# Kernel tuning notes

Hardware: AMD Instinct MI355X
Metric: run time of the kernel (lower is better)

Reference implementation:

```python
import jax, jax.numpy as jnp
import numpy as np

B, C, H, W, K = 2, 3, 256, 256, 51  # output H,W; filter size K; input is (H+K-1, W+K-1)


def _sepconv(inp, vertical, horizontal):
    # inp: [B,C,H+K-1,W+K-1]; vertical/horizontal: [B,K,H,W]
    Kf = vertical.shape[1]
    Ho, Wo = vertical.shape[2], vertical.shape[3]
    rows = jnp.stack([inp[:, :, i:i + Ho, :] for i in range(Kf)], axis=0)

    def body(acc, j):
        # window for horizontal offset j: [K,B,C,Ho,Wo]
        win = jax.lax.dynamic_slice_in_dim(rows, j, Wo, axis=4)
        # contract over vertical taps i with per-pixel vertical kernel
        vcon = jnp.einsum('kbchw,bkhw->bchw', win, vertical)
        # weight by per-pixel horizontal tap j and accumulate
        acc = acc + vcon * horizontal[:, j][:, None, :, :]
        return acc, None

    acc0 = jnp.zeros((inp.shape[0], inp.shape[1], Ho, Wo), inp.dtype)
    out, _ = jax.lax.scan(body, acc0, jnp.arange(Kf))
    return out


def setup_inputs() -> dict:
    key = jax.random.key(0)
    k1, k2, k3 = jax.random.split(key, 3)
    tenInput = jax.random.normal(k1, (B, C, H + K - 1, W + K - 1), dtype=jnp.float32)
    tenVertical = jax.random.normal(k2, (B, K, H, W), dtype=jnp.float32)
    tenHorizontal = jax.random.normal(k3, (B, K, H, W), dtype=jnp.float32)
    return {"tenInput": tenInput, "tenVertical": tenVertical, "tenHorizontal": tenHorizontal}


def reference(tenInput, tenVertical, tenHorizontal):
    return _sepconv(tenInput, tenVertical, tenHorizontal)
```

## Files before the change

kernel.cpp:

```cpp
#include <hip/hip_runtime.h>


namespace {
constexpr int KK = 51;
constexpr int NB = 2;
constexpr int NC = 3;
constexpr int HH = 256;
constexpr int WW = 256;
constexpr int IN_H = HH + KK - 1;
constexpr int IN_W = WW + KK - 1;

constexpr int TILE_W = 64;
constexpr int TILE_H = 8;
constexpr int NTX = 8;
constexpr int R = 8;
constexpr int NTY = 8;
constexpr int NS = 4;
constexpr int NTHREADS = NTX * NTY * NS;
constexpr int HALO_W = TILE_W + KK - 1;
constexpr int LDS_W = 116;
constexpr int LDS_H = TILE_H + KK - 1;
constexpr int KSTRIDE = HH * WW;
constexpr int HCH  = 4 * TILE_H * TILE_W;
constexpr int UNIT = 2 * HCH;
}

__device__ __forceinline__ float fget(const float4 v, int i) {
  return (i == 0) ? v.x : (i == 1) ? v.y : (i == 2) ? v.z : v.w;
}

template <int P, int JJ>
__device__ __forceinline__ void fma_jtap(const float4 (&v4)[4][2], const float4 (&w4)[4][3],
                                         const float4 ha, const float4 hb, float (&acc)[R]) {
#pragma unroll
  for (int rx = 0; rx < R; ++rx) {
    const int k  = rx + JJ;
    const int sl = (P + k / 4) % 3;
    const int cp = k & 3;
    const int vh = rx >> 2, vc = rx & 3;
    float tv = fget(v4[0][vh], vc) * fget(w4[0][sl], cp);
    tv = fmaf(fget(v4[1][vh], vc), fget(w4[1][sl], cp), tv);
    tv = fmaf(fget(v4[2][vh], vc), fget(w4[2][sl], cp), tv);
    tv = fmaf(fget(v4[3][vh], vc), fget(w4[3][sl], cp), tv);
    const float hv = (rx < 4) ? fget(ha, vc) : fget(hb, vc);
    acc[rx] = fmaf(hv, tv, acc[rx]);
  }
}

template <int P>
__device__ __forceinline__ void full_chunk(const float4 (&v4)[4][2], float4 (&w4)[4][3],
                                           const int (&woff)[4], int wcol,
                                           const float* hb, int off0, int off1,
                                           float (&acc)[R], const float* smem) {
  const float4 h0a = *reinterpret_cast<const float4*>(hb + off0);
  const float4 h0b = *reinterpret_cast<const float4*>(hb + off1);
  const float4 h1a = *reinterpret_cast<const float4*>(hb + 512 + off0);
  const float4 h1b = *reinterpret_cast<const float4*>(hb + 512 + off1);
  fma_jtap<P, 0>(v4, w4, h0a, h0b, acc);
  const float4 h2a = *reinterpret_cast<const float4*>(hb + 1024 + off0);
  const float4 h2b = *reinterpret_cast<const float4*>(hb + 1024 + off1);
  fma_jtap<P, 1>(v4, w4, h1a, h1b, acc);
  const float4 h3a = *reinterpret_cast<const float4*>(hb + 1536 + off0);
  const float4 h3b = *reinterpret_cast<const float4*>(hb + 1536 + off1);
  fma_jtap<P, 2>(v4, w4, h2a, h2b, acc);
  fma_jtap<P, 3>(v4, w4, h3a, h3b, acc);
#pragma unroll
  for (int ib = 0; ib < 4; ++ib)
    w4[ib][P] = *reinterpret_cast<const float4*>(&smem[woff[ib] + wcol]);
}

__global__ __launch_bounds__(NTHREADS, 1)
void sepconv_kernel(
    const float* __restrict__ inp,
    const float* __restrict__ vert,
    const float* __restrict__ horiz,
    float* __restrict__ out)
{
  __shared__ float lds[LDS_H * LDS_W];
  __shared__ float hbuf[2 * UNIT];

  const int tid = threadIdx.x;
  const int tx  = tid & (NTX - 1);
  const int ty  = (tid >> 3) & (NTY - 1);
  const int s   = tid >> 6;

  const int x0 = blockIdx.x * TILE_W;
  const int y0 = blockIdx.y * TILE_H;
  const int bc = blockIdx.z;
  const int b  = bc / NC;
  const int c  = bc % NC;

  {
    const float* src = inp + (((size_t)(b * NC + c)) * IN_H + y0) * IN_W + x0;
    constexpr int total2 = LDS_H * (HALO_W / 2);
    for (int e = tid; e < total2; e += NTHREADS) {
      const int col2 = e % (HALO_W / 2);
      const int r    = e / (HALO_W / 2);
      const float2 v = *reinterpret_cast<const float2*>(src + (size_t)r * IN_W + col2 * 2);
      float* dst = &lds[r * LDS_W + col2 * 2];
      dst[0] = v.x; dst[1] = v.y;
    }
  }

  const float* hblk = horiz + (((size_t)b * KK) * HH + y0) * WW + x0;
  int jj_[4], goff_[4], ldso_[4];
#pragma unroll
  for (int r = 0; r < 4; ++r) {
    const int p   = r * 256 + tid;
    const int rem = p & 127;
    const int row = rem >> 4;
    const int c4  = rem & 15;
    const int q   = (c4 - row) & 15;
    jj_[r]   = p >> 7;
    goff_[r] = row * WW + q * 4;
    ldso_[r] = (r * 256 + (tid & ~63)) * 4;
  }
  auto stage_full = [&](int jbase, int bufn) {
#pragma unroll
    for (int r = 0; r < 4; ++r) {
      const float* g = hblk + (size_t)(jbase + jj_[r]) * KSTRIDE + goff_[r];
      float* l = &hbuf[bufn * UNIT + ldso_[r]];
      __builtin_amdgcn_global_load_lds((const __attribute__((address_space(1))) void*)g,
                                       (__attribute__((address_space(3))) void*)l, 16, 0, 0);
    }
  };
  auto stage_half = [&](int bufn) {
#pragma unroll
    for (int r = 0; r < 2; ++r) {
      const int j  = 48 + jj_[r];
      const int jc = (j <= 50) ? j : 50;
      const float* g = hblk + (size_t)jc * KSTRIDE + goff_[r];
      float* l = &hbuf[bufn * UNIT + ldso_[r]];
      __builtin_amdgcn_global_load_lds((const __attribute__((address_space(1))) void*)g,
                                       (__attribute__((address_space(3))) void*)l, 16, 0, 0);
    }
  };

  stage_full(0, 0);
  __syncthreads();
  int buf = 0;
  int un  = 1;

  auto stage_next = [&]() {
    if (un < 6) stage_full(8 * un, buf ^ 1);
    else        stage_half(buf ^ 1);
    un = (un == 6) ? 0 : un + 1;
  };

  const int lx = tx * R;
  const int xg = x0 + lx;
  const int yg = y0 + ty;

  const int off0 = ty * 64 + ((2 * tx + ty) & 15) * 4;
  const int off1 = ty * 64 + ((2 * tx + 1 + ty) & 15) * 4;

  float acc[R];
#pragma unroll
  for (int rx = 0; rx < R; ++rx) acc[rx] = 0.f;

  const int blk0 = (s == 0) ? 0 : (3 * s + 1);
  const int nblk = (s == 0) ? 4 : 3;

  const float* vbase = vert + (((size_t)b * KK) * HH + yg) * WW + xg;

#pragma unroll 1
  for (int t = 0; t < 4; ++t) {
    const bool act = (t < nblk);
    float4 v4[4][2];
    float4 w4[4][3];
    int    woff[4];
    if (act) {
      const int ibase = (blk0 + t) * 4;
#pragma unroll
      for (int ib = 0; ib < 4; ++ib) {
        const int iv = ibase + ib;
        const int ic = (iv <= 50) ? iv : 50;
        float4 va = *reinterpret_cast<const float4*>(vbase + (size_t)ic * KSTRIDE);
        float4 vb = *reinterpret_cast<const float4*>(vbase + (size_t)ic * KSTRIDE + 4);
        if (iv > 50) { va = make_float4(0.f, 0.f, 0.f, 0.f); vb = va; }
        v4[ib][0] = va; v4[ib][1] = vb;
        woff[ib] = (ty + ic) * LDS_W;
        const float4* p = reinterpret_cast<const float4*>(&lds[woff[ib] + lx]);
        w4[ib][0] = p[0]; w4[ib][1] = p[1]; w4[ib][2] = p[2];
      }
    }

#pragma unroll 1
    for (int h2 = 0; h2 < 2; ++h2) {
      const int cb = lx + 24 * h2 + 12;
      const float* hb0;
      stage_next();
      hb0 = hbuf + buf * UNIT;
      if (act) {
        full_chunk<0>(v4, w4, woff, cb + 0, hb0,        off0, off1, acc, lds);
        full_chunk<1>(v4, w4, woff, cb + 4, hb0 + HCH,  off0, off1, acc, lds);
      }
      __syncthreads(); buf ^= 1;
      stage_next();
      hb0 = hbuf + buf * UNIT;
      if (act) {
        full_chunk<2>(v4, w4, woff, cb + 8,  hb0,       off0, off1, acc, lds);
        full_chunk<0>(v4, w4, woff, cb + 12, hb0 + HCH, off0, off1, acc, lds);
      }
      __syncthreads(); buf ^= 1;
      stage_next();
      hb0 = hbuf + buf * UNIT;
      if (act) {
        full_chunk<1>(v4, w4, woff, cb + 16, hb0,       off0, off1, acc, lds);
        full_chunk<2>(v4, w4, woff, cb + 20, hb0 + HCH, off0, off1, acc, lds);
      }
      __syncthreads(); buf ^= 1;
    }

    stage_next();
    if (act) {
      const float* hb = hbuf + buf * UNIT;
      const float4 e0a = *reinterpret_cast<const float4*>(hb + off0);
      const float4 e0b = *reinterpret_cast<const float4*>(hb + off1);
      const float4 e1a = *reinterpret_cast<const float4*>(hb + 512 + off0);
      const float4 e1b = *reinterpret_cast<const float4*>(hb + 512 + off1);
      const float4 e2a = *reinterpret_cast<const float4*>(hb + 1024 + off0);
      const float4 e2b = *reinterpret_cast<const float4*>(hb + 1024 + off1);
      fma_jtap<0, 0>(v4, w4, e0a, e0b, acc);
      fma_jtap<0, 1>(v4, w4, e1a, e1b, acc);
      fma_jtap<0, 2>(v4, w4, e2a, e2b, acc);
    }
    __syncthreads(); buf ^= 1;
  }

  if (s > 0) {
    float* p = &lds[((s - 1) * 64 + ty * NTX + tx) * R];
#pragma unroll
    for (int rx = 0; rx < R; ++rx) p[rx] = acc[rx];
  }
  __syncthreads();
  if (s == 0) {
#pragma unroll
    for (int g = 0; g < 3; ++g) {
      const float* p = &lds[(g * 64 + ty * NTX + tx) * R];
#pragma unroll
      for (int rx = 0; rx < R; ++rx) acc[rx] += p[rx];
    }
    float* o = out + (((size_t)(b * NC + c)) * HH + yg) * WW + xg;
    *reinterpret_cast<float4*>(o)     = make_float4(acc[0], acc[1], acc[2], acc[3]);
    *reinterpret_cast<float4*>(o + 4) = make_float4(acc[4], acc[5], acc[6], acc[7]);
  }
}

extern "C" void kernel_launch(void* const* d_in, const int* in_sizes, int n_in,
                              void* d_out, int out_size, void* d_ws, size_t ws_size,
                              hipStream_t stream) {
  const float* inp   = (const float*)d_in[0];
  const float* vert  = (const float*)d_in[1];
  const float* horiz = (const float*)d_in[2];
  float* out = (float*)d_out;

  dim3 grid(WW / TILE_W, HH / TILE_H, NB * NC);
  sepconv_kernel<<<grid, NTHREADS, 0, stream>>>(inp, vert, horiz, out);
}
```

Measured before the change: 151.1 us.

## Split vertical taps across two block halves and sum partials in second kernel

Result: no change. 149.8 us (-0.8%).

```diff
diff --git a/kernel.cpp b/kernel.cpp
--- a/kernel.cpp
+++ b/kernel.cpp
@@ -19,10 +19,11 @@
 constexpr int NTHREADS = NTX * NTY * NS;
 constexpr int HALO_W = TILE_W + KK - 1;
 constexpr int LDS_W = 116;
-constexpr int LDS_H = TILE_H + KK - 1;
+constexpr int LDS_H = 33;
 constexpr int KSTRIDE = HH * WW;
 constexpr int HCH  = 4 * TILE_H * TILE_W;
 constexpr int UNIT = 2 * HCH;
+constexpr int OUTN = NB * NC * HH * WW;
 }
 
 __device__ __forceinline__ float fget(const float4 v, int i) {
@@ -74,7 +75,7 @@
     const float* __restrict__ inp,
     const float* __restrict__ vert,
     const float* __restrict__ horiz,
-    float* __restrict__ out)
+    float* __restrict__ ws)
 {
   __shared__ float lds[LDS_H * LDS_W];
   __shared__ float hbuf[2 * UNIT];
@@ -86,17 +87,23 @@
 
   const int x0 = blockIdx.x * TILE_W;
   const int y0 = blockIdx.y * TILE_H;
-  const int bc = blockIdx.z;
+  const int zz = blockIdx.z;
+  const int bc = zz % (NB * NC);
+  const int half = zz / (NB * NC);
   const int b  = bc / NC;
   const int c  = bc % NC;
 
+  const int ROWBASE = half * 26;
+  const int ROWMAX  = half ? 50 : 25;
+
   {
-    const float* src = inp + (((size_t)(b * NC + c)) * IN_H + y0) * IN_W + x0;
+    const float* src = inp + (((size_t)(b * NC + c)) * IN_H) * IN_W + x0;
     constexpr int total2 = LDS_H * (HALO_W / 2);
     for (int e = tid; e < total2; e += NTHREADS) {
       const int col2 = e % (HALO_W / 2);
       const int r    = e / (HALO_W / 2);
-      const float2 v = *reinterpret_cast<const float2*>(src + (size_t)r * IN_W + col2 * 2);
+      const int gr   = min(y0 + ROWBASE + r, IN_H - 1);
+      const float2 v = *reinterpret_cast<const float2*>(src + (size_t)gr * IN_W + col2 * 2);
       float* dst = &lds[r * LDS_W + col2 * 2];
       dst[0] = v.x; dst[1] = v.y;
     }
@@ -158,28 +165,28 @@
 #pragma unroll
   for (int rx = 0; rx < R; ++rx) acc[rx] = 0.f;
 
-  const int blk0 = (s == 0) ? 0 : (3 * s + 1);
-  const int nblk = (s == 0) ? 4 : 3;
+  const int blk0 = (s < 3) ? 2 * s : 6;
+  const int nblk = (s < 3) ? 2 : 1;
 
   const float* vbase = vert + (((size_t)b * KK) * HH + yg) * WW + xg;
 
 #pragma unroll 1
-  for (int t = 0; t < 4; ++t) {
+  for (int t = 0; t < 2; ++t) {
     const bool act = (t < nblk);
     float4 v4[4][2];
     float4 w4[4][3];
     int    woff[4];
     if (act) {
-      const int ibase = (blk0 + t) * 4;
+      const int ibase = ROWBASE + (blk0 + t) * 4;
 #pragma unroll
       for (int ib = 0; ib < 4; ++ib) {
         const int iv = ibase + ib;
-        const int ic = (iv <= 50) ? iv : 50;
+        const int ic = (iv <= ROWMAX) ? iv : ROWMAX;
         float4 va = *reinterpret_cast<const float4*>(vbase + (size_t)ic * KSTRIDE);
         float4 vb = *reinterpret_cast<const float4*>(vbase + (size_t)ic * KSTRIDE + 4);
-        if (iv > 50) { va = make_float4(0.f, 0.f, 0.f, 0.f); vb = va; }
+        if (iv > ROWMAX) { va = make_float4(0.f, 0.f, 0.f, 0.f); vb = va; }
         v4[ib][0] = va; v4[ib][1] = vb;
-        woff[ib] = (ty + ic) * LDS_W;
+        woff[ib] = (ty + ic - ROWBASE) * LDS_W;
         const float4* p = reinterpret_cast<const float4*>(&lds[woff[ib] + lx]);
         w4[ib][0] = p[0]; w4[ib][1] = p[1]; w4[ib][2] = p[2];
       }
@@ -192,8 +199,8 @@
       stage_next();
       hb0 = hbuf + buf * UNIT;
       if (act) {
-        full_chunk<0>(v4, w4, woff, cb + 0, hb0,        off0, off1, acc, lds);
-        full_chunk<1>(v4, w4, woff, cb + 4, hb0 + HCH,  off0, off1, acc, lds);
+        full_chunk<0>(v4, w4, woff, cb + 0, hb0,       off0, off1, acc, lds);
+        full_chunk<1>(v4, w4, woff, cb + 4, hb0 + HCH, off0, off1, acc, lds);
       }
       __syncthreads(); buf ^= 1;
       stage_next();
@@ -241,10 +248,19 @@
 #pragma unroll
       for (int rx = 0; rx < R; ++rx) acc[rx] += p[rx];
     }
-    float* o = out + (((size_t)(b * NC + c)) * HH + yg) * WW + xg;
+    float* o = ws + (size_t)half * OUTN + (((size_t)(b * NC + c)) * HH + yg) * WW + xg;
     *reinterpret_cast<float4*>(o)     = make_float4(acc[0], acc[1], acc[2], acc[3]);
     *reinterpret_cast<float4*>(o + 4) = make_float4(acc[4], acc[5], acc[6], acc[7]);
   }
+}
+
+__global__ __launch_bounds__(256)
+void sum_halves(const float4* __restrict__ a, const float4* __restrict__ b,
+                float4* __restrict__ o)
+{
+  const int i = blockIdx.x * 256 + threadIdx.x;
+  const float4 x = a[i], y = b[i];
+  o[i] = make_float4(x.x + y.x, x.y + y.y, x.z + y.z, x.w + y.w);
 }
 
 extern "C" void kernel_launch(void* const* d_in, const int* in_sizes, int n_in,
@@ -254,7 +270,12 @@
   const float* vert  = (const float*)d_in[1];
   const float* horiz = (const float*)d_in[2];
   float* out = (float*)d_out;
-
-  dim3 grid(WW / TILE_W, HH / TILE_H, NB * NC);
-  sepconv_kernel<<<grid, NTHREADS, 0, stream>>>(inp, vert, horiz, out);
-}
+  float* ws  = (float*)d_ws;
+
+  dim3 grid(WW / TILE_W, HH / TILE_H, 2 * NB * NC);
+  sepconv_kernel<<<grid, NTHREADS, 0, stream>>>(inp, vert, horiz, ws);
+
+  const int n4 = OUTN / 4;
+  sum_halves<<<n4 / 256, 256, 0, stream>>>(
+      (const float4*)ws, (const float4*)(ws + OUTN), (float4*)out);
+}
```
